# Optimization experiments

Hardware: AMD Instinct MI355X
Metric: run time of the kernel (lower is better)

Reference implementation:

```python
import jax, jax.numpy as jnp
import numpy as np


def setup_inputs() -> dict:
    key = jax.random.key(0)
    k1, k2, k3 = jax.random.split(key, 3)
    B, N, F_in, F_out = 8, 2048, 128, 128
    x = jax.random.normal(k1, (B, N, F_in), dtype=jnp.float32)
    adj = jax.random.uniform(k2, (B, N, N), dtype=jnp.float32)
    W = jax.random.normal(k3, (F_out, F_in), dtype=jnp.float32) * (1.0 / np.sqrt(F_in))
    b = jnp.zeros((F_out,), dtype=jnp.float32)
    return {"x": x, "adj": adj, "W": W, "b": b}


def reference(x, adj, W, b):
    # adj: [B,N,N], x: [B,N,F]
    N = adj.shape[-1]
    adj = adj + jnp.eye(N, dtype=adj.dtype)  # add self-loops
    d_inv_sqrt = jnp.sum(adj, axis=-1) ** -0.5  # [B,N]
    # D^-1/2 A D^-1/2 as row/col broadcast scale (same math as diag bmm)
    adj_norm = d_inv_sqrt[:, :, None] * adj * d_inv_sqrt[:, None, :]
    out = jnp.einsum('bnm,bmf->bnf', adj_norm, x)  # aggregate
    out = jnp.einsum('bnf,of->bno', out, W) + b    # linear
    return out
```

## Files before the change

### kernel.cpp

```cpp
#include <hip/hip_runtime.h>
#include <hip/hip_bf16.h>

typedef __attribute__((ext_vector_type(8))) short s16x8;
typedef __attribute__((ext_vector_type(4))) float f32x4;

#define B_  8
#define N_  2048
#define F_  128
#define BM  32
#define BK  64
#define NT  (N_/BK)

__device__ __forceinline__ short bfc(float f) {
  __hip_bfloat16 h = __float2bfloat16(f);
  return __builtin_bit_cast(short, h);
}

__device__ __forceinline__ void gload16(const void* g, void* l) {
  __builtin_amdgcn_global_load_lds(
      (const __attribute__((address_space(1))) unsigned*)g,
      (__attribute__((address_space(3))) unsigned*)l, 16, 0, 0);
}

__global__ __launch_bounds__(256) void k_deg(const float* __restrict__ adj,
                                             float* __restrict__ dinv) {
  const int row  = blockIdx.x * 4 + (threadIdx.x >> 6);
  const int lane = threadIdx.x & 63;
  const float* p = adj + (size_t)row * N_;
  float s = 0.f;
#pragma unroll
  for (int it = 0; it < 8; ++it) {
    float4 v = *reinterpret_cast<const float4*>(p + it * 256 + lane * 4);
    s += (v.x + v.y) + (v.z + v.w);
  }
#pragma unroll
  for (int off = 32; off > 0; off >>= 1) s += __shfl_down(s, off);
  if (lane == 0) dinv[row] = 1.0f / sqrtf(s + 1.0f);
}

__global__ __launch_bounds__(256) void k_prep(const float* __restrict__ x,
                                              const float* __restrict__ dinv,
                                              unsigned short* __restrict__ xt) {
  __shared__ short s[F_ * 64];
  const int b  = blockIdx.x >> 5;
  const int t  = blockIdx.x & 31;
  const int rp = threadIdx.x >> 3;
  const int f0 = (threadIdx.x & 7) * 16;
  const int r0 = rp * 2;
  const float* x0 = x + ((size_t)(b * N_) + t * 64 + r0) * F_ + f0;
  const float d0 = dinv[b * N_ + t * 64 + r0];
  const float d1 = dinv[b * N_ + t * 64 + r0 + 1];
#pragma unroll
  for (int u = 0; u < 16; u += 4) {
    float4 v0 = *reinterpret_cast<const float4*>(x0 + u);
    float4 v1 = *reinterpret_cast<const float4*>(x0 + F_ + u);
    float a0[4] = {v0.x, v0.y, v0.z, v0.w};
    float a1[4] = {v1.x, v1.y, v1.z, v1.w};
#pragma unroll
    for (int j = 0; j < 4; ++j) {
      const int f = f0 + u + j;
      unsigned lo = (unsigned short)bfc(a0[j] * d0);
      unsigned hi = (unsigned short)bfc(a1[j] * d1);
      *reinterpret_cast<unsigned*>(&s[f * 64 + (r0 ^ ((f & 7) << 3))]) = lo | (hi << 16);
    }
  }
  __syncthreads();
  const s16x8* sp = reinterpret_cast<const s16x8*>(s);
  s16x8* op = reinterpret_cast<s16x8*>(xt + (size_t)blockIdx.x * 8192);
#pragma unroll
  for (int j = 0; j < 4; ++j) op[threadIdx.x * 4 + j] = sp[threadIdx.x * 4 + j];
}

__global__ __launch_bounds__(512, 4) void k_gcn(const float* __restrict__ adj,
                                                const float* __restrict__ x,
                                                const float* __restrict__ W,
                                                const float* __restrict__ bias,
                                                const float* __restrict__ dinv,
                                                const unsigned short* __restrict__ xt,
                                                float* __restrict__ out) {
  __shared__ short s_main[2 * BM * 64 + 2 * F_ * 64];
  __shared__ short s_w[F_ * 136];
  short* const sadj0 = s_main;
  short* const sadj1 = s_main + 2048;
  short* const sxt0  = s_main + 4096;
  short* const sxt1  = s_main + 12288;
  short* const s_o1  = s_main;

  const int tid  = threadIdx.x;
  const int lane = tid & 63;
  const int wv   = tid >> 6;
  const int wrow = wv & 1;
  const int wcol = wv >> 1;

  const int batch = blockIdx.x & 7;
  const int n0    = (blockIdx.x >> 3) * BM;

  {
    const int o   = tid >> 2;
    const int f0c = (tid & 3) * 32;
    const float* wp = W + o * F_ + f0c;
#pragma unroll
    for (int u = 0; u < 8; ++u) {
      float4 v = *reinterpret_cast<const float4*>(wp + u * 4);
      short4 h;
      h.x = bfc(v.x); h.y = bfc(v.y); h.z = bfc(v.z); h.w = bfc(v.w);
      *reinterpret_cast<short4*>(&s_w[o * 136 + f0c + u * 4]) = h;
    }
  }
  asm volatile("s_waitcnt vmcnt(0)" ::: "memory");
  __builtin_amdgcn_sched_barrier(0);

  const int ai = tid >> 4;
  const int aj = (tid & 15) * 4;
  const float* adj_row = adj + (size_t)(batch * N_ + n0 + ai) * N_ + aj;
  const int a_lds = ai * 64 + (aj ^ ((ai & 7) << 3));

  const unsigned short* xt_b = xt + (size_t)batch * NT * 8192;

  f32x4 acc[2] = {};
  float4 aA, aB;

  aA = *reinterpret_cast<const float4*>(adj_row);
  gload16(xt_b + tid * 8, sxt0 + tid * 8);
  gload16(xt_b + 4096 + tid * 8, sxt0 + 4096 + tid * 8);
  aB = *reinterpret_cast<const float4*>(adj_row + BK);

  auto step = [&](int t, float4& aCur, short* sadj_c, short* sxt_c, short* sxt_n) {
    {
      short4 h;
      h.x = bfc(aCur.x); h.y = bfc(aCur.y); h.z = bfc(aCur.z); h.w = bfc(aCur.w);
      *reinterpret_cast<short4*>(&sadj_c[a_lds]) = h;
    }
    if (t < NT - 1) asm volatile("s_waitcnt vmcnt(1) lgkmcnt(0)" ::: "memory");
    else            asm volatile("s_waitcnt vmcnt(0) lgkmcnt(0)" ::: "memory");
    __builtin_amdgcn_s_barrier();
    __builtin_amdgcn_sched_barrier(0);
    if (t + 1 < NT) {
      const unsigned short* src = xt_b + (size_t)(t + 1) * 8192;
      gload16(src + tid * 8, sxt_n + tid * 8);
      gload16(src + 4096 + tid * 8, sxt_n + 4096 + tid * 8);
      if (t + 2 < NT) aCur = *reinterpret_cast<const float4*>(adj_row + (t + 2) * BK);
    }
    {
      const int row  = wrow * 16 + (lane & 15);
      const int swzr = (row & 7) << 3;
      const int krun = (lane >> 4) * 8;
      const short* sa = sadj_c + row * 64;
      s16x8 a0 = *reinterpret_cast<const s16x8*>(sa + (krun ^ swzr));
      s16x8 a1 = *reinterpret_cast<const s16x8*>(sa + ((32 + krun) ^ swzr));
#pragma unroll
      for (int ct = 0; ct < 2; ++ct) {
        const int f    = wcol * 32 + ct * 16 + (lane & 15);
        const int swzf = (f & 7) << 3;
        const short* sb = sxt_c + f * 64;
        s16x8 b0 = *reinterpret_cast<const s16x8*>(sb + (krun ^ swzf));
        s16x8 b1 = *reinterpret_cast<const s16x8*>(sb + ((32 + krun) ^ swzf));
        acc[ct] = __builtin_amdgcn_mfma_f32_16x16x32_bf16(a0, b0, acc[ct], 0, 0, 0);
        acc[ct] = __builtin_amdgcn_mfma_f32_16x16x32_bf16(a1, b1, acc[ct], 0, 0, 0);
      }
    }
  };

#pragma unroll 1
  for (int tt = 0; tt < NT; tt += 2) {
    step(tt,     aA, sadj0, sxt0, sxt1);
    step(tt + 1, aB, sadj1, sxt1, sxt0);
  }

  __syncthreads();
  {
    const int lr4 = (lane >> 4) * 4;
    const int lc  = lane & 15;
#pragma unroll
    for (int r = 0; r < 4; ++r) {
      const int nl = wrow * 16 + lr4 + r;
      const float dn = dinv[batch * N_ + n0 + nl];
      const float* xrow = x + (size_t)(batch * N_ + n0 + nl) * F_;
#pragma unroll
      for (int ct = 0; ct < 2; ++ct) {
        const int f = wcol * 32 + ct * 16 + lc;
        s_o1[nl * 136 + f] = bfc(dn * acc[ct][r] + dn * dn * xrow[f]);
      }
    }
  }
  __syncthreads();

  f32x4 acc2[2] = {};
  {
    const int lc   = lane & 15;
    const int krun = (lane >> 4) * 8;
#pragma unroll
    for (int kk = 0; kk < 4; ++kk) {
      s16x8 af = *reinterpret_cast<const s16x8*>(&s_o1[(wrow * 16 + lc) * 136 + kk * 32 + krun]);
#pragma unroll
      for (int ot = 0; ot < 2; ++ot) {
        const int o = wcol * 32 + ot * 16 + lc;
        s16x8 bw = *reinterpret_cast<const s16x8*>(&s_w[o * 136 + kk * 32 + krun]);
        acc2[ot] = __builtin_amdgcn_mfma_f32_16x16x32_bf16(af, bw, acc2[ot], 0, 0, 0);
      }
    }
  }
  {
    const int lr4 = (lane >> 4) * 4;
    const int lc  = lane & 15;
#pragma unroll
    for (int ot = 0; ot < 2; ++ot) {
      const int o  = wcol * 32 + ot * 16 + lc;
      const float bb = bias[o];
#pragma unroll
      for (int r = 0; r < 4; ++r) {
        const int nl = wrow * 16 + lr4 + r;
        out[(size_t)(batch * N_ + n0 + nl) * F_ + o] = acc2[ot][r] + bb;
      }
    }
  }
}

__global__ __launch_bounds__(512) void k_gcn_fb(const float* __restrict__ adj,
                                                const float* __restrict__ x,
                                                const float* __restrict__ W,
                                                const float* __restrict__ bias,
                                                const float* __restrict__ dinv,
                                                float* __restrict__ out) {
  __shared__ short s_mem[64 * 72 + F_ * 72];
  __shared__ short s_w[F_ * 136];
  short* const s_adj = s_mem;
  short* const s_xb  = s_mem + 64 * 72;
  short* const s_o1  = s_mem;

  const int tid  = threadIdx.x;
  const int lane = tid & 63;
  const int wv   = tid >> 6;
  const int wrow = wv & 3;
  const int whal = wv >> 2;

  const int batch = blockIdx.x & 7;
  const int n0    = (blockIdx.x >> 3) * 64;

  {
    const int o  = tid >> 2;
    const int f0 = (tid & 3) * 32;
    const float* wp = W + o * F_ + f0;
#pragma unroll
    for (int u = 0; u < 8; ++u) {
      float4 v = *reinterpret_cast<const float4*>(wp + u * 4);
      short4 h;
      h.x = bfc(v.x); h.y = bfc(v.y); h.z = bfc(v.z); h.w = bfc(v.w);
      *reinterpret_cast<short4*>(&s_w[o * 136 + f0 + u * 4]) = h;
    }
  }

  const int ai  = tid >> 3;
  const int aj  = (tid & 7) * 8;
  const int xk2 = tid >> 4;
  const int xf0 = (tid & 15) * 8;

  const float* adj_row = adj + (size_t)(batch * N_ + n0 + ai) * N_;
  const float* x_b     = x + (size_t)batch * N_ * F_;
  const float* dv_b    = dinv + batch * N_;

  float4 ra0, ra1, rx0, rx1, rx2, rx3;
  float rd0, rd1;

  auto issue = [&](int k0) {
    ra0 = *reinterpret_cast<const float4*>(adj_row + k0 + aj);
    ra1 = *reinterpret_cast<const float4*>(adj_row + k0 + aj + 4);
    const float* xr = x_b + (size_t)(k0 + 2 * xk2) * F_ + xf0;
    rx0 = *reinterpret_cast<const float4*>(xr);
    rx1 = *reinterpret_cast<const float4*>(xr + 4);
    rx2 = *reinterpret_cast<const float4*>(xr + F_);
    rx3 = *reinterpret_cast<const float4*>(xr + F_ + 4);
    rd0 = dv_b[k0 + 2 * xk2];
    rd1 = dv_b[k0 + 2 * xk2 + 1];
  };

  f32x4 acc[4] = {};
  issue(0);
#pragma unroll 1
  for (int t = 0; t < N_ / 64; ++t) {
    __syncthreads();
    {
      s16x8 h;
      h[0] = bfc(ra0.x); h[1] = bfc(ra0.y); h[2] = bfc(ra0.z); h[3] = bfc(ra0.w);
      h[4] = bfc(ra1.x); h[5] = bfc(ra1.y); h[6] = bfc(ra1.z); h[7] = bfc(ra1.w);
      *reinterpret_cast<s16x8*>(&s_adj[ai * 72 + aj]) = h;
    }
    {
      float a0[8] = {rx0.x, rx0.y, rx0.z, rx0.w, rx1.x, rx1.y, rx1.z, rx1.w};
      float a1[8] = {rx2.x, rx2.y, rx2.z, rx2.w, rx3.x, rx3.y, rx3.z, rx3.w};
      const int kbase = (2 * xk2) ^ ((tid & 7) << 3);
#pragma unroll
      for (int u = 0; u < 8; ++u) {
        unsigned lo = (unsigned short)bfc(a0[u] * rd0);
        unsigned hi = (unsigned short)bfc(a1[u] * rd1);
        *reinterpret_cast<unsigned*>(&s_xb[(xf0 + u) * 72 + kbase]) = lo | (hi << 16);
      }
    }
    if (t + 1 < N_ / 64) issue((t + 1) * 64);
    __syncthreads();
    {
      const int arow = (wrow * 16 + (lane & 15)) * 72 + ((lane >> 4) * 8);
      s16x8 a0 = *reinterpret_cast<const s16x8*>(&s_adj[arow]);
      s16x8 a1 = *reinterpret_cast<const s16x8*>(&s_adj[arow + 32]);
      const int krun = (lane >> 4) * 8;
#pragma unroll
      for (int ct = 0; ct < 4; ++ct) {
        const int f   = whal * 64 + ct * 16 + (lane & 15);
        const int xsw = ((f >> 3) & 7) << 3;
        s16x8 b0 = *reinterpret_cast<const s16x8*>(&s_xb[f * 72 + (krun ^ xsw)]);
        s16x8 b1 = *reinterpret_cast<const s16x8*>(&s_xb[f * 72 + ((krun + 32) ^ xsw)]);
        acc[ct] = __builtin_amdgcn_mfma_f32_16x16x32_bf16(a0, b0, acc[ct], 0, 0, 0);
        acc[ct] = __builtin_amdgcn_mfma_f32_16x16x32_bf16(a1, b1, acc[ct], 0, 0, 0);
      }
    }
  }

  __syncthreads();
  {
    const int lr4 = (lane >> 4) * 4;
    const int lc  = lane & 15;
#pragma unroll
    for (int r = 0; r < 4; ++r) {
      const int nl = wrow * 16 + lr4 + r;
      const float dn = dv_b[n0 + nl];
      const float* xrow = x_b + (size_t)(n0 + nl) * F_;
#pragma unroll
      for (int ct = 0; ct < 4; ++ct) {
        const int f = whal * 64 + ct * 16 + lc;
        s_o1[nl * 136 + f] = bfc(dn * acc[ct][r] + dn * dn * xrow[f]);
      }
    }
  }
  __syncthreads();

  f32x4 acc2[4] = {};
  {
    const int lc   = lane & 15;
    const int krun = (lane >> 4) * 8;
#pragma unroll
    for (int kk = 0; kk < 4; ++kk) {
      s16x8 af = *reinterpret_cast<const s16x8*>(&s_o1[(wrow * 16 + lc) * 136 + kk * 32 + krun]);
#pragma unroll
      for (int ot = 0; ot < 4; ++ot) {
        const int o = whal * 64 + ot * 16 + lc;
        s16x8 bf8 = *reinterpret_cast<const s16x8*>(&s_w[o * 136 + kk * 32 + krun]);
        acc2[ot] = __builtin_amdgcn_mfma_f32_16x16x32_bf16(af, bf8, acc2[ot], 0, 0, 0);
      }
    }
  }
  {
    const int lr4 = (lane >> 4) * 4;
    const int lc  = lane & 15;
#pragma unroll
    for (int ot = 0; ot < 4; ++ot) {
      const int o  = whal * 64 + ot * 16 + lc;
      const float bb = bias[o];
#pragma unroll
      for (int r = 0; r < 4; ++r) {
        const int nl = wrow * 16 + lr4 + r;
        out[(size_t)(batch * N_ + n0 + nl) * F_ + o] = acc2[ot][r] + bb;
      }
    }
  }
}

extern "C" void kernel_launch(void* const* d_in, const int* in_sizes, int n_in,
                              void* d_out, int out_size, void* d_ws, size_t ws_size,
                              hipStream_t stream) {
  const float* x   = (const float*)d_in[0];
  const float* adj = (const float*)d_in[1];
  const float* W   = (const float*)d_in[2];
  const float* b   = (const float*)d_in[3];
  float* outp = (float*)d_out;
  float* dinv = (float*)d_ws;
  unsigned short* xt = (unsigned short*)((char*)d_ws + 65536);

  k_deg<<<(B_ * N_) / 4, 256, 0, stream>>>(adj, dinv);
  if (ws_size >= 65536 + (size_t)B_ * NT * 8192 * 2) {
    k_prep<<<B_ * NT, 256, 0, stream>>>(x, dinv, xt);
    k_gcn<<<B_ * (N_ / BM), 512, 0, stream>>>(adj, x, W, b, dinv, xt, outp);
  } else {
    k_gcn_fb<<<B_ * (N_ / 64), 512, 0, stream>>>(adj, x, W, b, dinv, outp);
  }
}
```

Baseline: 58.24 us.

## Fuse degree pass with bf16 swizzled adjacency pre-conversion and triple-buffer main GEMM

The degree kernel now also adds the self-loop and writes a bf16, tile-ordered, pre-swizzled copy of the adjacency. The main kernel streams these bf16 tiles straight into LDS with async loads using a three-stage buffer ring, and keeps W fragments in registers instead of LDS. This removes the fp32-to-bf16 conversion and register staging from the main loop. The cost is an extra 64MB write plus reread of the bf16 copy, and it needs a large workspace.

```diff
diff --git a/kernel.cpp b/kernel.cpp
--- a/kernel.cpp
+++ b/kernel.cpp
@@ -10,6 +10,11 @@
 #define BM  32
 #define BK  64
 #define NT  (N_/BK)
+#define NRB (N_/BM)
+
+#define WS_XT   (65536)
+#define WS_ADJB ((size_t)8 << 20)
+#define ADJB_BYTES ((size_t)B_ * NRB * NT * 4096)
 
 __device__ __forceinline__ short bfc(float f) {
   __hip_bfloat16 h = __float2bfloat16(f);
@@ -21,21 +26,42 @@
       (const __attribute__((address_space(1))) unsigned*)g,
       (__attribute__((address_space(3))) unsigned*)l, 16, 0, 0);
 }
-
-__global__ __launch_bounds__(256) void k_deg(const float* __restrict__ adj,
-                                             float* __restrict__ dinv) {
-  const int row  = blockIdx.x * 4 + (threadIdx.x >> 6);
-  const int lane = threadIdx.x & 63;
-  const float* p = adj + (size_t)row * N_;
+__device__ __forceinline__ void gload4(const void* g, void* l) {
+  __builtin_amdgcn_global_load_lds(
+      (const __attribute__((address_space(1))) unsigned*)g,
+      (__attribute__((address_space(3))) unsigned*)l, 4, 0, 0);
+}
+
+__global__ __launch_bounds__(256) void k_pass1(const float* __restrict__ adj,
+                                               float* __restrict__ dinv,
+                                               unsigned short* __restrict__ adjb) {
+  const int b  = blockIdx.x >> 7;
+  const int r0 = (blockIdx.x & 127) * 16;
+  const int rl = threadIdx.x >> 4;
+  const int j  = threadIdx.x & 15;
+  const int r  = r0 + rl;
+  const int c0 = j * 4;
+  const float* row = adj + ((size_t)b * N_ + r) * N_;
+  const int rb  = r >> 5;
+  const int rit = r & 31;
+  unsigned short* tb0 = adjb + ((size_t)(b * NRB + rb) * NT) * 2048 + rit * 64;
+  const int swz = (r & 7) << 3;
+  const int cs  = c0 ^ swz;
+
   float s = 0.f;
-#pragma unroll
-  for (int it = 0; it < 8; ++it) {
-    float4 v = *reinterpret_cast<const float4*>(p + it * 256 + lane * 4);
+#pragma unroll 4
+  for (int t = 0; t < NT; ++t) {
+    const int cg = t * BK + c0;
+    float4 v = *reinterpret_cast<const float4*>(row + cg);
+    if (r >= cg && r < cg + 4) (&v.x)[r - cg] += 1.0f;
     s += (v.x + v.y) + (v.z + v.w);
-  }
-#pragma unroll
-  for (int off = 32; off > 0; off >>= 1) s += __shfl_down(s, off);
-  if (lane == 0) dinv[row] = 1.0f / sqrtf(s + 1.0f);
+    short4 h;
+    h.x = bfc(v.x); h.y = bfc(v.y); h.z = bfc(v.z); h.w = bfc(v.w);
+    *reinterpret_cast<short4*>(tb0 + (size_t)t * 2048 + cs) = h;
+  }
+  s += __shfl_xor(s, 1); s += __shfl_xor(s, 2);
+  s += __shfl_xor(s, 4); s += __shfl_xor(s, 8);
+  if (j == 0) dinv[b * N_ + r] = 1.0f / sqrtf(s);
 }
 
 __global__ __launch_bounds__(256) void k_prep(const float* __restrict__ x,
@@ -57,10 +83,10 @@
     float a0[4] = {v0.x, v0.y, v0.z, v0.w};
     float a1[4] = {v1.x, v1.y, v1.z, v1.w};
 #pragma unroll
-    for (int j = 0; j < 4; ++j) {
-      const int f = f0 + u + j;
-      unsigned lo = (unsigned short)bfc(a0[j] * d0);
-      unsigned hi = (unsigned short)bfc(a1[j] * d1);
+    for (int k = 0; k < 4; ++k) {
+      const int f = f0 + u + k;
+      unsigned lo = (unsigned short)bfc(a0[k] * d0);
+      unsigned hi = (unsigned short)bfc(a1[k] * d1);
       *reinterpret_cast<unsigned*>(&s[f * 64 + (r0 ^ ((f & 7) << 3))]) = lo | (hi << 16);
     }
   }
@@ -68,23 +94,18 @@
   const s16x8* sp = reinterpret_cast<const s16x8*>(s);
   s16x8* op = reinterpret_cast<s16x8*>(xt + (size_t)blockIdx.x * 8192);
 #pragma unroll
-  for (int j = 0; j < 4; ++j) op[threadIdx.x * 4 + j] = sp[threadIdx.x * 4 + j];
-}
-
-__global__ __launch_bounds__(512, 4) void k_gcn(const float* __restrict__ adj,
-                                                const float* __restrict__ x,
-                                                const float* __restrict__ W,
-                                                const float* __restrict__ bias,
-                                                const float* __restrict__ dinv,
-                                                const unsigned short* __restrict__ xt,
-                                                float* __restrict__ out) {
-  __shared__ short s_main[2 * BM * 64 + 2 * F_ * 64];
-  __shared__ short s_w[F_ * 136];
-  short* const sadj0 = s_main;
-  short* const sadj1 = s_main + 2048;
-  short* const sxt0  = s_main + 4096;
-  short* const sxt1  = s_main + 12288;
-  short* const s_o1  = s_main;
+  for (int k = 0; k < 4; ++k) op[threadIdx.x * 4 + k] = sp[threadIdx.x * 4 + k];
+}
+
+__global__ __launch_bounds__(512, 4) void k_gcn3(const unsigned short* __restrict__ adjb,
+                                                 const unsigned short* __restrict__ xt,
+                                                 const float* __restrict__ W,
+                                                 const float* __restrict__ bias,
+                                                 const float* __restrict__ dinv,
+                                                 float* __restrict__ out) {
+  __shared__ short s_adj[3 * 2048];
+  __shared__ short s_xt[3 * 8192];
+  short* const s_o1 = s_xt;
 
   const int tid  = threadIdx.x;
   const int lane = tid & 63;
@@ -93,78 +114,79 @@
   const int wcol = wv >> 1;
 
   const int batch = blockIdx.x & 7;
-  const int n0    = (blockIdx.x >> 3) * BM;
-
-  {
-    const int o   = tid >> 2;
-    const int f0c = (tid & 3) * 32;
-    const float* wp = W + o * F_ + f0c;
-#pragma unroll
-    for (int u = 0; u < 8; ++u) {
-      float4 v = *reinterpret_cast<const float4*>(wp + u * 4);
-      short4 h;
-      h.x = bfc(v.x); h.y = bfc(v.y); h.z = bfc(v.z); h.w = bfc(v.w);
-      *reinterpret_cast<short4*>(&s_w[o * 136 + f0c + u * 4]) = h;
+  const int rb    = blockIdx.x >> 3;
+  const int n0    = rb * BM;
+
+  s16x8 wfr[2][4];
+#pragma unroll
+  for (int ot = 0; ot < 2; ++ot) {
+#pragma unroll
+    for (int kk = 0; kk < 4; ++kk) {
+      const int o  = wcol * 32 + ot * 16 + (lane & 15);
+      const int f0 = kk * 32 + (lane >> 4) * 8;
+      float4 v0 = *reinterpret_cast<const float4*>(W + o * F_ + f0);
+      float4 v1 = *reinterpret_cast<const float4*>(W + o * F_ + f0 + 4);
+      s16x8 h;
+      h[0] = bfc(v0.x); h[1] = bfc(v0.y); h[2] = bfc(v0.z); h[3] = bfc(v0.w);
+      h[4] = bfc(v1.x); h[5] = bfc(v1.y); h[6] = bfc(v1.z); h[7] = bfc(v1.w);
+      wfr[ot][kk] = h;
     }
   }
   asm volatile("s_waitcnt vmcnt(0)" ::: "memory");
   __builtin_amdgcn_sched_barrier(0);
 
-  const int ai = tid >> 4;
-  const int aj = (tid & 15) * 4;
-  const float* adj_row = adj + (size_t)(batch * N_ + n0 + ai) * N_ + aj;
-  const int a_lds = ai * 64 + (aj ^ ((ai & 7) << 3));
-
-  const unsigned short* xt_b = xt + (size_t)batch * NT * 8192;
+  const unsigned short* atile = adjb + ((size_t)(batch * NRB + rb) * NT) * 2048;
+  const unsigned short* xtb   = xt + (size_t)batch * NT * 8192;
+
+  auto issueX = [&](int t, int buf) {
+    const unsigned short* src = xtb + (size_t)t * 8192;
+    short* dst = s_xt + buf * 8192;
+    gload16(src + tid * 8, dst + tid * 8);
+    gload16(src + 4096 + tid * 8, dst + 4096 + tid * 8);
+  };
+  auto issueA = [&](int t, int buf) {
+    const unsigned short* src = atile + (size_t)t * 2048;
+    short* dst = s_adj + buf * 2048;
+    gload4(src + tid * 2, dst + tid * 2);
+    gload4(src + 1024 + tid * 2, dst + 1024 + tid * 2);
+  };
 
   f32x4 acc[2] = {};
-  float4 aA, aB;
-
-  aA = *reinterpret_cast<const float4*>(adj_row);
-  gload16(xt_b + tid * 8, sxt0 + tid * 8);
-  gload16(xt_b + 4096 + tid * 8, sxt0 + 4096 + tid * 8);
-  aB = *reinterpret_cast<const float4*>(adj_row + BK);
-
-  auto step = [&](int t, float4& aCur, short* sadj_c, short* sxt_c, short* sxt_n) {
-    {
-      short4 h;
-      h.x = bfc(aCur.x); h.y = bfc(aCur.y); h.z = bfc(aCur.z); h.w = bfc(aCur.w);
-      *reinterpret_cast<short4*>(&sadj_c[a_lds]) = h;
-    }
-    if (t < NT - 1) asm volatile("s_waitcnt vmcnt(1) lgkmcnt(0)" ::: "memory");
-    else            asm volatile("s_waitcnt vmcnt(0) lgkmcnt(0)" ::: "memory");
+
+  issueX(0, 0); issueA(0, 0);
+  issueX(1, 1); issueA(1, 1);
+
+  int bc = 0;
+#pragma unroll 1
+  for (int t = 0; t < NT; ++t) {
+    if (t < NT - 1) asm volatile("s_waitcnt vmcnt(4)" ::: "memory");
+    else            asm volatile("s_waitcnt vmcnt(0)" ::: "memory");
     __builtin_amdgcn_s_barrier();
     __builtin_amdgcn_sched_barrier(0);
-    if (t + 1 < NT) {
-      const unsigned short* src = xt_b + (size_t)(t + 1) * 8192;
-      gload16(src + tid * 8, sxt_n + tid * 8);
-      gload16(src + 4096 + tid * 8, sxt_n + 4096 + tid * 8);
-      if (t + 2 < NT) aCur = *reinterpret_cast<const float4*>(adj_row + (t + 2) * BK);
+    if (t + 2 < NT) {
+      int bn = bc + 2; if (bn >= 3) bn -= 3;
+      issueX(t + 2, bn);
+      issueA(t + 2, bn);
     }
     {
+      const short* sa = &s_adj[bc * 2048];
+      const short* sx = &s_xt[bc * 8192];
       const int row  = wrow * 16 + (lane & 15);
       const int swzr = (row & 7) << 3;
       const int krun = (lane >> 4) * 8;
-      const short* sa = sadj_c + row * 64;
-      s16x8 a0 = *reinterpret_cast<const s16x8*>(sa + (krun ^ swzr));
-      s16x8 a1 = *reinterpret_cast<const s16x8*>(sa + ((32 + krun) ^ swzr));
+      s16x8 a0 = *reinterpret_cast<const s16x8*>(sa + row * 64 + (krun ^ swzr));
+      s16x8 a1 = *reinterpret_cast<const s16x8*>(sa + row * 64 + ((32 + krun) ^ swzr));
 #pragma unroll
       for (int ct = 0; ct < 2; ++ct) {
         const int f    = wcol * 32 + ct * 16 + (lane & 15);
         const int swzf = (f & 7) << 3;
-        const short* sb = sxt_c + f * 64;
-        s16x8 b0 = *reinterpret_cast<const s16x8*>(sb + (krun ^ swzf));
-        s16x8 b1 = *reinterpret_cast<const s16x8*>(sb + ((32 + krun) ^ swzf));
+        s16x8 b0 = *reinterpret_cast<const s16x8*>(sx + f * 64 + (krun ^ swzf));
+        s16x8 b1 = *reinterpret_cast<const s16x8*>(sx + f * 64 + ((32 + krun) ^ swzf));
         acc[ct] = __builtin_amdgcn_mfma_f32_16x16x32_bf16(a0, b0, acc[ct], 0, 0, 0);
         acc[ct] = __builtin_amdgcn_mfma_f32_16x16x32_bf16(a1, b1, acc[ct], 0, 0, 0);
       }
     }
-  };
-
-#pragma unroll 1
-  for (int tt = 0; tt < NT; tt += 2) {
-    step(tt,     aA, sadj0, sxt0, sxt1);
-    step(tt + 1, aB, sadj1, sxt1, sxt0);
+    bc = (bc + 1 == 3) ? 0 : bc + 1;
   }
 
   __syncthreads();
@@ -175,11 +197,10 @@
     for (int r = 0; r < 4; ++r) {
       const int nl = wrow * 16 + lr4 + r;
       const float dn = dinv[batch * N_ + n0 + nl];
-      const float* xrow = x + (size_t)(batch * N_ + n0 + nl) * F_;
 #pragma unroll
       for (int ct = 0; ct < 2; ++ct) {
         const int f = wcol * 32 + ct * 16 + lc;
-        s_o1[nl * 136 + f] = bfc(dn * acc[ct][r] + dn * dn * xrow[f]);
+        s_o1[nl * 136 + f] = bfc(dn * acc[ct][r]);
       }
     }
   }
@@ -193,11 +214,8 @@
     for (int kk = 0; kk < 4; ++kk) {
       s16x8 af = *reinterpret_cast<const s16x8*>(&s_o1[(wrow * 16 + lc) * 136 + kk * 32 + krun]);
 #pragma unroll
-      for (int ot = 0; ot < 2; ++ot) {
-        const int o = wcol * 32 + ot * 16 + lc;
-        s16x8 bw = *reinterpret_cast<const s16x8*>(&s_w[o * 136 + kk * 32 + krun]);
-        acc2[ot] = __builtin_amdgcn_mfma_f32_16x16x32_bf16(af, bw, acc2[ot], 0, 0, 0);
-      }
+      for (int ot = 0; ot < 2; ++ot)
+        acc2[ot] = __builtin_amdgcn_mfma_f32_16x16x32_bf16(af, wfr[ot][kk], acc2[ot], 0, 0, 0);
     }
   }
   {
@@ -214,6 +232,22 @@
       }
     }
   }
+}
+
+__global__ __launch_bounds__(256) void k_deg(const float* __restrict__ adj,
+                                             float* __restrict__ dinv) {
+  const int row  = blockIdx.x * 4 + (threadIdx.x >> 6);
+  const int lane = threadIdx.x & 63;
+  const float* p = adj + (size_t)row * N_;
+  float s = 0.f;
+#pragma unroll
+  for (int it = 0; it < 8; ++it) {
+    float4 v = *reinterpret_cast<const float4*>(p + it * 256 + lane * 4);
+    s += (v.x + v.y) + (v.z + v.w);
+  }
+#pragma unroll
+  for (int off = 32; off > 0; off >>= 1) s += __shfl_down(s, off);
+  if (lane == 0) dinv[row] = 1.0f / sqrtf(s + 1.0f);
 }
 
 __global__ __launch_bounds__(512) void k_gcn_fb(const float* __restrict__ adj,
@@ -373,13 +407,15 @@
   const float* b   = (const float*)d_in[3];
   float* outp = (float*)d_out;
   float* dinv = (float*)d_ws;
-  unsigned short* xt = (unsigned short*)((char*)d_ws + 65536);
-
-  k_deg<<<(B_ * N_) / 4, 256, 0, stream>>>(adj, dinv);
-  if (ws_size >= 65536 + (size_t)B_ * NT * 8192 * 2) {
+  unsigned short* xt   = (unsigned short*)((char*)d_ws + WS_XT);
+  unsigned short* adjb = (unsigned short*)((char*)d_ws + WS_ADJB);
+
+  if (ws_size >= WS_ADJB + ADJB_BYTES) {
+    k_pass1<<<B_ * (N_ / 16), 256, 0, stream>>>(adj, dinv, adjb);
     k_prep<<<B_ * NT, 256, 0, stream>>>(x, dinv, xt);
-    k_gcn<<<B_ * (N_ / BM), 512, 0, stream>>>(adj, x, W, b, dinv, xt, outp);
+    k_gcn3<<<B_ * NRB, 512, 0, stream>>>(adjb, xt, W, b, dinv, outp);
   } else {
+    k_deg<<<(B_ * N_) / 4, 256, 0, stream>>>(adj, dinv);
     k_gcn_fb<<<B_ * (N_ / 64), 512, 0, stream>>>(adj, x, W, b, dinv, outp);
   }
 }
```

Result: slower. 78.68 us (+35.1%).
